# Optimization experiments

Measured on AMD Instinct MI355X. Metric: run time of the kernel, lower is better.

The kernel has to match this reference:

```python
import jax, jax.numpy as jnp
import numpy as np

B, SQ, SK, D, H = 8, 1024, 1024, 1024, 16
DH = D // H  # attention head size = 64
LN_EPS = 1e-5


def _layer_norm(x, g, b):
    m = jnp.mean(x, axis=-1, keepdims=True)
    v = jnp.mean(jnp.square(x - m), axis=-1, keepdims=True)
    return (x - m) * jax.lax.rsqrt(v + LN_EPS) * g + b


def setup_inputs() -> dict:
    key = jax.random.key(0)
    ks = jax.random.split(key, 12)
    s = 0.02
    return {
        "hidden_states": jax.random.normal(ks[0], (B, SQ, D), jnp.float32),
        "context": jax.random.normal(ks[1], (B, SK, D), jnp.float32),
        "Wq": jax.random.normal(ks[2], (D, D), jnp.float32) * s,
        "bq": jnp.zeros((D,), jnp.float32),
        "Wk": jax.random.normal(ks[3], (D, D), jnp.float32) * s,
        "bk": jnp.zeros((D,), jnp.float32),
        "Wv": jax.random.normal(ks[4], (D, D), jnp.float32) * s,
        "bv": jnp.zeros((D,), jnp.float32),
        "Wobs": jax.random.normal(ks[5], (D, D), jnp.float32) * s,
        "bobs": jnp.zeros((D,), jnp.float32),
        "Wmat": jax.random.normal(ks[6], (D, D), jnp.float32) * s,
        "bmat": jnp.zeros((D,), jnp.float32),
        "ln_g": jnp.ones((D,), jnp.float32),
        "ln_b": jnp.zeros((D,), jnp.float32),
    }


def reference(hidden_states, context, Wq, bq, Wk, bk, Wv, bv,
              Wobs, bobs, Wmat, bmat, ln_g, ln_b):
    # QKV projections (torch Linear: x @ W.T + b)
    q = hidden_states @ Wq.T + bq            # [B, SQ, D]
    k = context @ Wk.T + bk                  # [B, SK, D]
    v = context @ Wv.T + bv                  # [B, SK, D]

    # ---- Guide_Block: single-head SDPA over full D, then linear->ReLU->LN ----
    # (dropout is identity in eval mode)
    score = jnp.einsum('bqd,bkd->bqk', q, k) / np.sqrt(D)   # [B, SQ, SK]
    attn = jax.nn.softmax(score, axis=-1)
    gctx = jnp.einsum('bqk,bkd->bqd', attn, v)              # [B, SQ, D]
    new_q = _layer_norm(jax.nn.relu(gctx @ Wobs.T + bobs), ln_g, ln_b)
    new_k = _layer_norm(jax.nn.relu(k @ Wmat.T + bmat), ln_g, ln_b)

    # ---- Multi-head attention with guided q/k and original v ----
    qh = new_q.reshape(B, SQ, H, DH).transpose(0, 2, 1, 3)  # [B, H, SQ, DH]
    kh = new_k.reshape(B, SK, H, DH).transpose(0, 2, 1, 3)
    vh = v.reshape(B, SK, H, DH).transpose(0, 2, 1, 3)
    scores = jnp.einsum('bhqd,bhkd->bhqk', qh, kh) / np.sqrt(DH)
    probs = jax.nn.softmax(scores, axis=-1)                 # attn dropout = identity (eval)
    out = jnp.einsum('bhqk,bhkd->bhqd', probs, vh)          # [B, H, SQ, DH]
    return out.transpose(0, 2, 1, 3).reshape(B, SQ, D)
```

## Files before the change

kernel.cpp:

```cpp
#include <hip/hip_runtime.h>
#include <hip/hip_bf16.h>

#define DEV __device__ __forceinline__

using bf16x8 = __attribute__((ext_vector_type(8))) short;
using f32x4  = __attribute__((ext_vector_type(4))) float;

#define MFMA16(a, b, c) __builtin_amdgcn_mfma_f32_16x16x32_bf16((a), (b), (c), 0, 0, 0)

#define GLOAD_LDS16(gp, lp)                                                        \
  __builtin_amdgcn_global_load_lds(                                               \
      (__attribute__((address_space(1))) unsigned int*)(gp),                      \
      (__attribute__((address_space(3))) unsigned int*)(lp), 16, 0, 0)

DEV float b2f(unsigned short u) {
  union { float f; unsigned u; } x; x.u = ((unsigned)u) << 16; return x.f;
}
DEV unsigned short f2b(float f) {
  union { float f; unsigned u; } x; x.f = f;
  unsigned r = x.u + 0x7FFFu + ((x.u >> 16) & 1u);
  return (unsigned short)(r >> 16);
}
DEV unsigned short f2b_trunc(float f) {
  union { float f; unsigned u; } x; x.f = f;
  return (unsigned short)(x.u >> 16);
}

__global__ __launch_bounds__(256) void detect_kernel(
    const unsigned short* __restrict__ hs, int* __restrict__ flag) {
  __shared__ int red[4];
  const int t = threadIdx.x;
  const ushort4* p = (const ushort4*)hs;
  int cnt = 0;
#pragma unroll
  for (int j = 0; j < 16; j++) {
    ushort4 u = p[j * 256 + t];
    cnt += (((u.x >> 7) & 0xFF) == 0xFF) + (((u.y >> 7) & 0xFF) == 0xFF) +
           (((u.z >> 7) & 0xFF) == 0xFF) + (((u.w >> 7) & 0xFF) == 0xFF);
  }
#pragma unroll
  for (int off = 32; off >= 1; off >>= 1) cnt += __shfl_xor(cnt, off, 64);
  if ((t & 63) == 0) red[t >> 6] = cnt;
  __syncthreads();
  if (t == 0) flag[0] = (red[0] + red[1] + red[2] + red[3] >= 4) ? 1 : 0;
}

__global__ __launch_bounds__(256) void convert2_kernel(
    const void* __restrict__ s0, const void* __restrict__ s1,
    unsigned short* __restrict__ d0, unsigned short* __restrict__ d1,
    const int* __restrict__ flag) {
  const int bid = blockIdx.x;
  const void* src;
  unsigned short* dst;
  long off;
  if (bid < 8192) { src = s0; dst = d0; off = (long)bid * 1024; }
  else            { src = s1; dst = d1; off = (long)(bid - 8192) * 1024; }
  const long i = off + threadIdx.x * 4;
  ushort4 o;
  if (*flag) {
    float4 f = ((const float4*)src)[i >> 2];
    o.x = f2b(f.x); o.y = f2b(f.y); o.z = f2b(f.z); o.w = f2b(f.w);
  } else {
    o = ((const ushort4*)src)[i >> 2];
  }
  ((ushort4*)dst)[i >> 2] = o;
}

__global__ __launch_bounds__(256) void convert_w_kernel(
    const void* __restrict__ s0, const void* __restrict__ s1,
    const void* __restrict__ s2, const void* __restrict__ s3,
    const void* __restrict__ s4, unsigned short* __restrict__ dst,
    const int* __restrict__ flag) {
  const void* srcs[5] = {s0, s1, s2, s3, s4};
  const void* src = srcs[blockIdx.y];
  unsigned short* d = dst + (long)blockIdx.y * 1048576;
  const int i = (blockIdx.x * 256 + threadIdx.x) * 4;
  ushort4 o;
  if (*flag) {
    float4 f = ((const float4*)src)[i >> 2];
    o.x = f2b(f.x); o.y = f2b(f.y); o.z = f2b(f.z); o.w = f2b(f.w);
  } else {
    o = ((const ushort4*)src)[i >> 2];
  }
  ((ushort4*)d)[i >> 2] = o;
}

__global__ __launch_bounds__(256) void convert_vec_kernel(
    const void* __restrict__ s0, const void* __restrict__ s1,
    const void* __restrict__ s2, const void* __restrict__ s3,
    const void* __restrict__ s4, const void* __restrict__ s5,
    const void* __restrict__ s6, unsigned short* __restrict__ dst,
    const int* __restrict__ flag) {
  const void* srcs[7] = {s0, s1, s2, s3, s4, s5, s6};
  const void* src = srcs[blockIdx.x];
  unsigned short* d = dst + blockIdx.x * 1024;
  const int i = threadIdx.x * 4;
  ushort4 o;
  if (*flag) {
    float4 f = ((const float4*)src)[i >> 2];
    o.x = f2b(f.x); o.y = f2b(f.y); o.z = f2b(f.z); o.w = f2b(f.w);
  } else {
    o = ((const ushort4*)src)[i >> 2];
  }
  ((ushort4*)d)[i >> 2] = o;
}

template <int RELU, int OUTBF16, int BIAS, int SPLIT>
__global__ __launch_bounds__(256, 2) void gemm_bt_kernel(
    const unsigned short* __restrict__ A, const unsigned short* __restrict__ B,
    const unsigned short* __restrict__ bias, void* __restrict__ Cv,
    void* __restrict__ Cv2, int M, int N, int K, long sA_, long sB_, long sC_,
    float scale) {
  __shared__ unsigned short sA[2][128 * 32];
  __shared__ unsigned short sB[2][128 * 32];
  const int t = threadIdx.x;
  const int wave = t >> 6, lane = t & 63;
  const int quad = lane >> 4, col = lane & 15;
  const int wm = wave >> 1, wn = wave & 1;
  const long zb = blockIdx.z;
  const unsigned short* Ab = A + zb * sA_ + (long)blockIdx.x * 128 * K;
  const unsigned short* Bb = B + zb * sB_ + (long)blockIdx.y * 128 * K;
  const int r0 = t >> 2;
  const int c0 = (t & 3) * 8;

  f32x4 zz = {0.f, 0.f, 0.f, 0.f};
  f32x4 acc[4][4];
#pragma unroll
  for (int i = 0; i < 4; i++)
#pragma unroll
    for (int j = 0; j < 4; j++) acc[i][j] = zz;

  for (int k0 = 0; k0 < K; k0 += 64) {
    __syncthreads();
#pragma unroll
    for (int p = 0; p < 2; p++) {
      GLOAD_LDS16(Ab + (long)r0 * K + k0 + p * 32 + c0,        &sA[p][t * 8]);
      GLOAD_LDS16(Ab + (long)(64 + r0) * K + k0 + p * 32 + c0, &sA[p][2048 + t * 8]);
      GLOAD_LDS16(Bb + (long)r0 * K + k0 + p * 32 + c0,        &sB[p][t * 8]);
      GLOAD_LDS16(Bb + (long)(64 + r0) * K + k0 + p * 32 + c0, &sB[p][2048 + t * 8]);
    }
    __syncthreads();
#pragma unroll
    for (int p = 0; p < 2; p++) {
      bf16x8 af[4], bfr[4];
#pragma unroll
      for (int mi = 0; mi < 4; mi++)
        af[mi] = *(const bf16x8*)&sA[p][(wm * 64 + mi * 16 + col) * 32 + quad * 8];
#pragma unroll
      for (int ni = 0; ni < 4; ni++)
        bfr[ni] = *(const bf16x8*)&sB[p][(wn * 64 + ni * 16 + col) * 32 + quad * 8];
#pragma unroll
      for (int mi = 0; mi < 4; mi++)
#pragma unroll
        for (int ni = 0; ni < 4; ni++)
          acc[mi][ni] = MFMA16(af[mi], bfr[ni], acc[mi][ni]);
    }
  }

  const int Rm = blockIdx.x * 128 + wm * 64;
  const int Cn = blockIdx.y * 128 + wn * 64;
  float bs[4];
#pragma unroll
  for (int ni = 0; ni < 4; ni++)
    bs[ni] = BIAS ? b2f(bias[Cn + ni * 16 + col]) : 0.f;

  unsigned short* Cb = (unsigned short*)Cv;
  int Nw = N, cadj = 0;
  if (SPLIT) {
    Nw = N >> 1;
    if (blockIdx.y >= (gridDim.y >> 1)) { Cb = (unsigned short*)Cv2; cadj = Nw; }
  }
#pragma unroll
  for (int mi = 0; mi < 4; mi++)
#pragma unroll
    for (int ni = 0; ni < 4; ni++)
#pragma unroll
      for (int r = 0; r < 4; r++) {
        int rr = Rm + mi * 16 + quad * 4 + r;
        int cc = Cn + ni * 16 + col;
        float v = acc[mi][ni][r] * scale + bs[ni];
        if (RELU) v = fmaxf(v, 0.f);
        if (OUTBF16)
          Cb[zb * sC_ + (long)rr * Nw + (cc - cadj)] = f2b(v);
        else
          ((float*)Cv)[zb * sC_ + (long)rr * N + cc] = v;
      }
}

__global__ __launch_bounds__(256) void softmax_kernel(
    const float* __restrict__ S, unsigned short* __restrict__ P) {
  __shared__ float red[8];
  const long row = blockIdx.x;
  const int t = threadIdx.x;
  const float4 v4 = ((const float4*)(S + row * 1024))[t];
  float x[4] = {v4.x, v4.y, v4.z, v4.w};
  float m = fmaxf(fmaxf(x[0], x[1]), fmaxf(x[2], x[3]));
#pragma unroll
  for (int off = 32; off >= 1; off >>= 1) m = fmaxf(m, __shfl_xor(m, off, 64));
  if ((t & 63) == 0) red[t >> 6] = m;
  __syncthreads();
  m = fmaxf(fmaxf(red[0], red[1]), fmaxf(red[2], red[3]));
  float e[4], s = 0.f;
#pragma unroll
  for (int i = 0; i < 4; i++) { e[i] = __expf(x[i] - m); s += e[i]; }
#pragma unroll
  for (int off = 32; off >= 1; off >>= 1) s += __shfl_xor(s, off, 64);
  __syncthreads();
  if ((t & 63) == 0) red[4 + (t >> 6)] = s;
  __syncthreads();
  s = red[4] + red[5] + red[6] + red[7];
  float inv = 1.f / s;
  ushort4 o;
  o.x = f2b(e[0] * inv); o.y = f2b(e[1] * inv);
  o.z = f2b(e[2] * inv); o.w = f2b(e[3] * inv);
  ((ushort4*)(P + row * 1024))[t] = o;
}

DEV float block_sum(float v, float* red, int t) {
#pragma unroll
  for (int off = 32; off >= 1; off >>= 1) v += __shfl_xor(v, off, 64);
  __syncthreads();
  if ((t & 63) == 0) red[t >> 6] = v;
  __syncthreads();
  return red[0] + red[1] + red[2] + red[3];
}

__global__ __launch_bounds__(256) void layernorm2_kernel(
    const unsigned short* __restrict__ X0, const unsigned short* __restrict__ X1,
    const unsigned short* __restrict__ G, const unsigned short* __restrict__ Bt,
    unsigned short* __restrict__ Y0, unsigned short* __restrict__ Y1) {
  __shared__ float red[4];
  const int bid = blockIdx.x;
  const unsigned short* X;
  unsigned short* Y;
  if (bid < 8192) { X = X0 + (long)bid * 1024; Y = Y0 + (long)bid * 1024; }
  else { X = X1 + (long)(bid - 8192) * 1024; Y = Y1 + (long)(bid - 8192) * 1024; }
  const int t = threadIdx.x;
  ushort4 u = ((const ushort4*)X)[t];
  float x[4] = {b2f(u.x), b2f(u.y), b2f(u.z), b2f(u.w)};
  float s = x[0] + x[1] + x[2] + x[3];
  float mean = block_sum(s, red, t) * (1.f / 1024.f);
  float d0 = x[0] - mean, d1 = x[1] - mean, d2 = x[2] - mean, d3 = x[3] - mean;
  float vs = d0 * d0 + d1 * d1 + d2 * d2 + d3 * d3;
  float var = block_sum(vs, red, t) * (1.f / 1024.f);
  float rs = rsqrtf(var + 1e-5f);
  ushort4 gu = ((const ushort4*)G)[t];
  ushort4 bu = ((const ushort4*)Bt)[t];
  ushort4 o;
  o.x = f2b(d0 * rs * b2f(gu.x) + b2f(bu.x));
  o.y = f2b(d1 * rs * b2f(gu.y) + b2f(bu.y));
  o.z = f2b(d2 * rs * b2f(gu.z) + b2f(bu.z));
  o.w = f2b(d3 * rs * b2f(gu.w) + b2f(bu.w));
  ((ushort4*)Y)[t] = o;
}

__global__ __launch_bounds__(256) void transpose_kernel(
    const unsigned short* __restrict__ V, unsigned short* __restrict__ VT) {
  __shared__ unsigned short tile[32][33];
  const int b = blockIdx.z;
  const int d0 = blockIdx.x * 32, sk0 = blockIdx.y * 32;
  const int tx = threadIdx.x & 31, ty = threadIdx.x >> 5;
#pragma unroll
  for (int i = 0; i < 32; i += 8)
    tile[ty + i][tx] = V[((long)(b * 1024 + sk0 + ty + i)) * 1024 + d0 + tx];
  __syncthreads();
#pragma unroll
  for (int i = 0; i < 32; i += 8)
    VT[((long)(b * 1024 + d0 + ty + i)) * 1024 + sk0 + tx] = tile[tx][ty + i];
}

__global__ __launch_bounds__(256, 2) void flash_mha_kernel(
    const unsigned short* __restrict__ Q, const unsigned short* __restrict__ K,
    const unsigned short* __restrict__ VT, void* __restrict__ O,
    const int* __restrict__ flag) {
  __shared__ unsigned short sK[2][2][32 * 32];
  __shared__ unsigned short sV[2][64 * 32];
  __shared__ unsigned short sP[4][32 * 32];
  const int t = threadIdx.x;
  const int wave = t >> 6, lane = t & 63;
  const int quad = lane >> 4, col = lane & 15;
  const int b = blockIdx.z, h = blockIdx.y;
  const int q0 = blockIdx.x * 128 + wave * 32;

  const int h2 = t >> 7, i7 = t & 127;
  const unsigned short* Ksrc =
      K + ((long)(b * 1024 + (i7 >> 2))) * 1024 + h * 64 + h2 * 32 + (i7 & 3) * 8;
  const unsigned short* Vsrc =
      VT + ((long)(b * 1024 + h * 64 + (t >> 2))) * 1024 + (t & 3) * 8;

  bf16x8 aq[2][2];
  {
    const unsigned short* qp =
        Q + ((long)(b * 1024 + q0 + col)) * 1024 + h * 64 + quad * 8;
    aq[0][0] = *(const bf16x8*)(qp);
    aq[0][1] = *(const bf16x8*)(qp + 32);
    aq[1][0] = *(const bf16x8*)(qp + 16 * 1024);
    aq[1][1] = *(const bf16x8*)(qp + 16 * 1024 + 32);
  }

  const f32x4 zz = {0.f, 0.f, 0.f, 0.f};
  f32x4 o[2][4], l[2];
#pragma unroll
  for (int mt = 0; mt < 2; mt++) {
    l[mt] = zz;
#pragma unroll
    for (int n = 0; n < 4; n++) o[mt][n] = zz;
  }
  bf16x8 ones;
#pragma unroll
  for (int i = 0; i < 8; i++) ones[i] = (short)0x3F80;

#define STAGE_KV(bi, kv0)                                             \
  {                                                                   \
    GLOAD_LDS16(Ksrc + (long)(kv0) * 1024, &sK[bi][h2][i7 * 8]);      \
    GLOAD_LDS16(Vsrc + (kv0), &sV[bi][t * 8]);                        \
  }

  STAGE_KV(0, 0);
  unsigned short* pw = &sP[wave][0];
  for (int kt = 0; kt < 32; kt++) {
    const int bi = kt & 1;
    __syncthreads();
    if (kt < 31) STAGE_KV(bi ^ 1, (kt + 1) * 32);

    bf16x8 kf[2][2];
#pragma unroll
    for (int nt = 0; nt < 2; nt++)
#pragma unroll
      for (int kh = 0; kh < 2; kh++)
        kf[nt][kh] = *(const bf16x8*)&sK[bi][kh][(nt * 16 + col) * 32 + quad * 8];
    f32x4 s[2][2];
#pragma unroll
    for (int mt = 0; mt < 2; mt++)
#pragma unroll
      for (int nt = 0; nt < 2; nt++) {
        s[mt][nt] = MFMA16(aq[mt][0], kf[nt][0], zz);
        s[mt][nt] = MFMA16(aq[mt][1], kf[nt][1], s[mt][nt]);
      }
#pragma unroll
    for (int mt = 0; mt < 2; mt++)
#pragma unroll
      for (int nt = 0; nt < 2; nt++)
#pragma unroll
        for (int r = 0; r < 4; r++) {
          float p = __expf(s[mt][nt][r] * 0.125f);
          pw[(mt * 16 + quad * 4 + r) * 32 + nt * 16 + col] = f2b_trunc(p);
        }
    __asm__ __volatile__("s_waitcnt lgkmcnt(0)" ::: "memory");
    bf16x8 ap[2];
#pragma unroll
    for (int mt = 0; mt < 2; mt++)
      ap[mt] = *(const bf16x8*)&pw[(mt * 16 + col) * 32 + quad * 8];
#pragma unroll
    for (int mt = 0; mt < 2; mt++) l[mt] = MFMA16(ap[mt], ones, l[mt]);
    bf16x8 vf[4];
#pragma unroll
    for (int n = 0; n < 4; n++)
      vf[n] = *(const bf16x8*)&sV[bi][(n * 16 + col) * 32 + quad * 8];
#pragma unroll
    for (int mt = 0; mt < 2; mt++)
#pragma unroll
      for (int n = 0; n < 4; n++) o[mt][n] = MFMA16(ap[mt], vf[n], o[mt][n]);
  }
#undef STAGE_KV

  const int f32o = *flag;
#pragma unroll
  for (int mt = 0; mt < 2; mt++)
#pragma unroll
    for (int r = 0; r < 4; r++) {
      float inv = 1.f / l[mt][r];
      const long base =
          ((long)(b * 1024 + q0 + mt * 16 + quad * 4 + r)) * 1024 + h * 64 + col;
      if (f32o) {
        float* Of = (float*)O;
#pragma unroll
        for (int n = 0; n < 4; n++) Of[base + n * 16] = o[mt][n][r] * inv;
      } else {
        unsigned short* Ou = (unsigned short*)O;
#pragma unroll
        for (int n = 0; n < 4; n++) Ou[base + n * 16] = f2b(o[mt][n][r] * inv);
      }
    }
}

extern "C" void kernel_launch(void* const* d_in, const int* in_sizes, int n_in,
                              void* d_out, int out_size, void* d_ws,
                              size_t ws_size, hipStream_t stream) {
  (void)in_sizes; (void)n_in; (void)out_size; (void)ws_size;
  const void* hs   = d_in[0];
  const void* ctx  = d_in[1];
  const void* Wq   = d_in[2];
  const void* bq   = d_in[3];
  const void* Wk   = d_in[4];
  const void* bk   = d_in[5];
  const void* Wv   = d_in[6];
  const void* bv   = d_in[7];
  const void* Wobs = d_in[8];
  const void* bobs = d_in[9];
  const void* Wmat = d_in[10];
  const void* bmat = d_in[11];
  const void* lng  = d_in[12];
  const void* lnb  = d_in[13];

  const long E = 8LL * 1024 * 1024;
  const long W1 = 1024L * 1024L;
  unsigned short* base = (unsigned short*)d_ws;
  unsigned short* hsb   = base;
  unsigned short* ctxb  = base + E;
  unsigned short* Wb    = base + 2 * E;
  unsigned short* Wqb   = Wb;
  unsigned short* Wkb   = Wb + W1;
  unsigned short* Wvb   = Wb + 2 * W1;
  unsigned short* Wobsb = Wb + 3 * W1;
  unsigned short* Wmatb = Wb + 4 * W1;
  unsigned short* vecs  = base + 2 * E + 5 * W1;
  unsigned short* bqb   = vecs;
  unsigned short* bkb   = vecs + 1024;
  unsigned short* bvb   = vecs + 2048;
  unsigned short* bobsb = vecs + 3072;
  unsigned short* bmatb = vecs + 4096;
  unsigned short* lngb  = vecs + 5120;
  unsigned short* lnbb  = vecs + 6144;
  int* flag = (int*)(vecs + 32768);
  unsigned short* q     = vecs + W1;
  unsigned short* k     = q + E;
  unsigned short* v     = k + E;
  unsigned short* vT    = v + E;
  float* scores = (float*)(vT + E);
  unsigned short* nq    = (unsigned short*)scores;
  unsigned short* newq  = ((unsigned short*)scores) + E;
  unsigned short* probs = hsb;
  unsigned short* gctx  = ctxb;
  unsigned short* nk    = v;
  unsigned short* newk  = q;

  dim3 blk(256);
  const long S1 = 1024L * 1024L;

  detect_kernel<<<dim3(1), blk, 0, stream>>>((const unsigned short*)hs, flag);
  convert2_kernel<<<dim3(16384), blk, 0, stream>>>(hs, ctx, hsb, ctxb, flag);
  convert_w_kernel<<<dim3(1024, 5), blk, 0, stream>>>(Wq, Wk, Wv, Wobs, Wmat, Wb, flag);
  convert_vec_kernel<<<dim3(7), blk, 0, stream>>>(bq, bk, bv, bobs, bmat, lng, lnb,
                                                  vecs, flag);

  gemm_bt_kernel<0, 1, 1, 0><<<dim3(64, 8, 1), blk, 0, stream>>>(
      hsb, Wqb, bqb, q, q, 8192, 1024, 1024, 0, 0, 0, 1.f);
  gemm_bt_kernel<0, 1, 1, 1><<<dim3(64, 16, 1), blk, 0, stream>>>(
      ctxb, Wkb, bkb, k, v, 8192, 2048, 1024, 0, 0, 0, 1.f);
  transpose_kernel<<<dim3(32, 32, 8), blk, 0, stream>>>(v, vT);
  gemm_bt_kernel<0, 0, 0, 0><<<dim3(8, 8, 8), blk, 0, stream>>>(
      q, k, nullptr, scores, scores, 1024, 1024, 1024, S1, S1, S1, 0.03125f);
  softmax_kernel<<<dim3(8192), blk, 0, stream>>>(scores, probs);
  gemm_bt_kernel<0, 1, 0, 0><<<dim3(8, 8, 8), blk, 0, stream>>>(
      probs, vT, nullptr, gctx, gctx, 1024, 1024, 1024, S1, S1, S1, 1.f);
  gemm_bt_kernel<1, 1, 1, 0><<<dim3(64, 8, 1), blk, 0, stream>>>(
      gctx, Wobsb, bobsb, nq, nq, 8192, 1024, 1024, 0, 0, 0, 1.f);
  gemm_bt_kernel<1, 1, 1, 0><<<dim3(64, 8, 1), blk, 0, stream>>>(
      k, Wmatb, bmatb, nk, nk, 8192, 1024, 1024, 0, 0, 0, 1.f);
  layernorm2_kernel<<<dim3(16384), blk, 0, stream>>>(nq, nk, lngb, lnbb, newq, newk);
  flash_mha_kernel<<<dim3(8, 16, 8), blk, 0, stream>>>(
      newq, newk, vT, d_out, flag);
}
```

Baseline: 405.4 us.

## Compute V transposed directly via swapped GEMM and widen flash MHA query tile

The separate V projection and transpose kernel are replaced by a GEMM that computes W_v·ctx^T, writing V^T per batch with a row-wise bias, which removes one full read and write pass over V. The flash multi-head attention kernel now handles 64 query rows per wave (256 per block) instead of 32, so each staged K/V tile is reused across twice as many queries. The P scratch buffer gets padded rows. The cost is higher register pressure in the flash kernel and half as many blocks, which may lower occupancy. The GEMM template is also reworked into mode-based epilogues.

```diff
diff --git a/kernel.cpp b/kernel.cpp
--- a/kernel.cpp
+++ b/kernel.cpp
@@ -105,12 +105,11 @@
   ((ushort4*)d)[i >> 2] = o;
 }
 
-template <int RELU, int OUTBF16, int BIAS, int SPLIT>
+template <int MODE>
 __global__ __launch_bounds__(256, 2) void gemm_bt_kernel(
     const unsigned short* __restrict__ A, const unsigned short* __restrict__ B,
-    const unsigned short* __restrict__ bias, void* __restrict__ Cv,
-    void* __restrict__ Cv2, int M, int N, int K, long sA_, long sB_, long sC_,
-    float scale) {
+    const void* __restrict__ aux, void* __restrict__ Cv,
+    int M, int N, int K, long sA_, long sB_, long sC_, float scale) {
   __shared__ unsigned short sA[2][128 * 32];
   __shared__ unsigned short sB[2][128 * 32];
   const int t = threadIdx.x;
@@ -159,32 +158,39 @@
 
   const int Rm = blockIdx.x * 128 + wm * 64;
   const int Cn = blockIdx.y * 128 + wn * 64;
-  float bs[4];
-#pragma unroll
-  for (int ni = 0; ni < 4; ni++)
-    bs[ni] = BIAS ? b2f(bias[Cn + ni * 16 + col]) : 0.f;
-
-  unsigned short* Cb = (unsigned short*)Cv;
-  int Nw = N, cadj = 0;
-  if (SPLIT) {
-    Nw = N >> 1;
-    if (blockIdx.y >= (gridDim.y >> 1)) { Cb = (unsigned short*)Cv2; cadj = Nw; }
-  }
-#pragma unroll
-  for (int mi = 0; mi < 4; mi++)
+  float bs[4] = {0.f, 0.f, 0.f, 0.f};
+  if (MODE == 0 || MODE == 1) {
 #pragma unroll
     for (int ni = 0; ni < 4; ni++)
+      bs[ni] = b2f(((const unsigned short*)aux)[Cn + ni * 16 + col]);
+  }
+#pragma unroll
+  for (int mi = 0; mi < 4; mi++) {
+    float rowf[4];
+#pragma unroll
+    for (int r = 0; r < 4; r++) {
+      const int rr = Rm + mi * 16 + quad * 4 + r;
+      rowf[r] = (MODE == 4) ? b2f(((const unsigned short*)aux)[rr]) : 0.f;
+    }
+#pragma unroll
+    for (int ni = 0; ni < 4; ni++)
 #pragma unroll
       for (int r = 0; r < 4; r++) {
-        int rr = Rm + mi * 16 + quad * 4 + r;
-        int cc = Cn + ni * 16 + col;
-        float v = acc[mi][ni][r] * scale + bs[ni];
-        if (RELU) v = fmaxf(v, 0.f);
-        if (OUTBF16)
-          Cb[zb * sC_ + (long)rr * Nw + (cc - cadj)] = f2b(v);
+        const int rr = Rm + mi * 16 + quad * 4 + r;
+        const int cc = Cn + ni * 16 + col;
+        float v = acc[mi][ni][r] * scale;
+        if (MODE == 0 || MODE == 1) v += bs[ni];
+        if (MODE == 1) v = fmaxf(v, 0.f);
+        if (MODE == 4) v += rowf[r];
+        if (MODE == 2)
+          ((float*)Cv)[zb * sC_ + (long)rr * N + cc] = v;
+        else if (MODE == 4)
+          ((unsigned short*)Cv)[(long)(cc >> 10) * 1048576 + (long)rr * 1024 +
+                                (cc & 1023)] = f2b(v);
         else
-          ((float*)Cv)[zb * sC_ + (long)rr * N + cc] = v;
+          ((unsigned short*)Cv)[zb * sC_ + (long)rr * N + cc] = f2b(v);
       }
+  }
 }
 
 __global__ __launch_bounds__(256) void softmax_kernel(
@@ -254,33 +260,18 @@
   ((ushort4*)Y)[t] = o;
 }
 
-__global__ __launch_bounds__(256) void transpose_kernel(
-    const unsigned short* __restrict__ V, unsigned short* __restrict__ VT) {
-  __shared__ unsigned short tile[32][33];
-  const int b = blockIdx.z;
-  const int d0 = blockIdx.x * 32, sk0 = blockIdx.y * 32;
-  const int tx = threadIdx.x & 31, ty = threadIdx.x >> 5;
-#pragma unroll
-  for (int i = 0; i < 32; i += 8)
-    tile[ty + i][tx] = V[((long)(b * 1024 + sk0 + ty + i)) * 1024 + d0 + tx];
-  __syncthreads();
-#pragma unroll
-  for (int i = 0; i < 32; i += 8)
-    VT[((long)(b * 1024 + d0 + ty + i)) * 1024 + sk0 + tx] = tile[tx][ty + i];
-}
-
 __global__ __launch_bounds__(256, 2) void flash_mha_kernel(
     const unsigned short* __restrict__ Q, const unsigned short* __restrict__ K,
     const unsigned short* __restrict__ VT, void* __restrict__ O,
     const int* __restrict__ flag) {
   __shared__ unsigned short sK[2][2][32 * 32];
   __shared__ unsigned short sV[2][64 * 32];
-  __shared__ unsigned short sP[4][32 * 32];
+  __shared__ unsigned short sP[4][64 * 40];
   const int t = threadIdx.x;
   const int wave = t >> 6, lane = t & 63;
   const int quad = lane >> 4, col = lane & 15;
   const int b = blockIdx.z, h = blockIdx.y;
-  const int q0 = blockIdx.x * 128 + wave * 32;
+  const int q0 = blockIdx.x * 256 + wave * 64;
 
   const int h2 = t >> 7, i7 = t & 127;
   const unsigned short* Ksrc =
@@ -288,20 +279,21 @@
   const unsigned short* Vsrc =
       VT + ((long)(b * 1024 + h * 64 + (t >> 2))) * 1024 + (t & 3) * 8;
 
-  bf16x8 aq[2][2];
+  bf16x8 aq[4][2];
   {
     const unsigned short* qp =
         Q + ((long)(b * 1024 + q0 + col)) * 1024 + h * 64 + quad * 8;
-    aq[0][0] = *(const bf16x8*)(qp);
-    aq[0][1] = *(const bf16x8*)(qp + 32);
-    aq[1][0] = *(const bf16x8*)(qp + 16 * 1024);
-    aq[1][1] = *(const bf16x8*)(qp + 16 * 1024 + 32);
+#pragma unroll
+    for (int mt = 0; mt < 4; mt++) {
+      aq[mt][0] = *(const bf16x8*)(qp + (long)mt * 16 * 1024);
+      aq[mt][1] = *(const bf16x8*)(qp + (long)mt * 16 * 1024 + 32);
+    }
   }
 
   const f32x4 zz = {0.f, 0.f, 0.f, 0.f};
-  f32x4 o[2][4], l[2];
-#pragma unroll
-  for (int mt = 0; mt < 2; mt++) {
+  f32x4 o[4][4], l[4];
+#pragma unroll
+  for (int mt = 0; mt < 4; mt++) {
     l[mt] = zz;
 #pragma unroll
     for (int n = 0; n < 4; n++) o[mt][n] = zz;
@@ -329,36 +321,36 @@
 #pragma unroll
       for (int kh = 0; kh < 2; kh++)
         kf[nt][kh] = *(const bf16x8*)&sK[bi][kh][(nt * 16 + col) * 32 + quad * 8];
-    f32x4 s[2][2];
-#pragma unroll
-    for (int mt = 0; mt < 2; mt++)
+    f32x4 s[4][2];
+#pragma unroll
+    for (int mt = 0; mt < 4; mt++)
 #pragma unroll
       for (int nt = 0; nt < 2; nt++) {
         s[mt][nt] = MFMA16(aq[mt][0], kf[nt][0], zz);
         s[mt][nt] = MFMA16(aq[mt][1], kf[nt][1], s[mt][nt]);
       }
 #pragma unroll
-    for (int mt = 0; mt < 2; mt++)
+    for (int mt = 0; mt < 4; mt++)
 #pragma unroll
       for (int nt = 0; nt < 2; nt++)
 #pragma unroll
         for (int r = 0; r < 4; r++) {
           float p = __expf(s[mt][nt][r] * 0.125f);
-          pw[(mt * 16 + quad * 4 + r) * 32 + nt * 16 + col] = f2b_trunc(p);
+          pw[(mt * 16 + quad * 4 + r) * 40 + nt * 16 + col] = f2b_trunc(p);
         }
     __asm__ __volatile__("s_waitcnt lgkmcnt(0)" ::: "memory");
-    bf16x8 ap[2];
-#pragma unroll
-    for (int mt = 0; mt < 2; mt++)
-      ap[mt] = *(const bf16x8*)&pw[(mt * 16 + col) * 32 + quad * 8];
-#pragma unroll
-    for (int mt = 0; mt < 2; mt++) l[mt] = MFMA16(ap[mt], ones, l[mt]);
+    bf16x8 ap[4];
+#pragma unroll
+    for (int mt = 0; mt < 4; mt++)
+      ap[mt] = *(const bf16x8*)&pw[(mt * 16 + col) * 40 + quad * 8];
+#pragma unroll
+    for (int mt = 0; mt < 4; mt++) l[mt] = MFMA16(ap[mt], ones, l[mt]);
     bf16x8 vf[4];
 #pragma unroll
     for (int n = 0; n < 4; n++)
       vf[n] = *(const bf16x8*)&sV[bi][(n * 16 + col) * 32 + quad * 8];
 #pragma unroll
-    for (int mt = 0; mt < 2; mt++)
+    for (int mt = 0; mt < 4; mt++)
 #pragma unroll
       for (int n = 0; n < 4; n++) o[mt][n] = MFMA16(ap[mt], vf[n], o[mt][n]);
   }
@@ -366,7 +358,7 @@
 
   const int f32o = *flag;
 #pragma unroll
-  for (int mt = 0; mt < 2; mt++)
+  for (int mt = 0; mt < 4; mt++)
 #pragma unroll
     for (int r = 0; r < 4; r++) {
       float inv = 1.f / l[mt][r];
@@ -425,15 +417,16 @@
   int* flag = (int*)(vecs + 32768);
   unsigned short* q     = vecs + W1;
   unsigned short* k     = q + E;
-  unsigned short* v     = k + E;
-  unsigned short* vT    = v + E;
-  float* scores = (float*)(vT + E);
-  unsigned short* nq    = (unsigned short*)scores;
-  unsigned short* newq  = ((unsigned short*)scores) + E;
+  unsigned short* vT    = k + E;
+  unsigned short* N1    = vT + E;
+  unsigned short* N2    = N1 + E;
+  float* scores = (float*)(N2 + E);
   unsigned short* probs = hsb;
   unsigned short* gctx  = ctxb;
-  unsigned short* nk    = v;
-  unsigned short* newk  = q;
+  unsigned short* nq    = N1;
+  unsigned short* nk    = q;
+  unsigned short* newq  = (unsigned short*)scores;
+  unsigned short* newk  = N2;
 
   dim3 blk(256);
   const long S1 = 1024L * 1024L;
@@ -444,21 +437,22 @@
   convert_vec_kernel<<<dim3(7), blk, 0, stream>>>(bq, bk, bv, bobs, bmat, lng, lnb,
                                                   vecs, flag);
 
-  gemm_bt_kernel<0, 1, 1, 0><<<dim3(64, 8, 1), blk, 0, stream>>>(
-      hsb, Wqb, bqb, q, q, 8192, 1024, 1024, 0, 0, 0, 1.f);
-  gemm_bt_kernel<0, 1, 1, 1><<<dim3(64, 16, 1), blk, 0, stream>>>(
-      ctxb, Wkb, bkb, k, v, 8192, 2048, 1024, 0, 0, 0, 1.f);
-  transpose_kernel<<<dim3(32, 32, 8), blk, 0, stream>>>(v, vT);
-  gemm_bt_kernel<0, 0, 0, 0><<<dim3(8, 8, 8), blk, 0, stream>>>(
-      q, k, nullptr, scores, scores, 1024, 1024, 1024, S1, S1, S1, 0.03125f);
+  gemm_bt_kernel<0><<<dim3(64, 8, 1), blk, 0, stream>>>(
+      hsb, Wqb, bqb, q, 8192, 1024, 1024, 0, 0, 0, 1.f);
+  gemm_bt_kernel<0><<<dim3(64, 8, 1), blk, 0, stream>>>(
+      ctxb, Wkb, bkb, k, 8192, 1024, 1024, 0, 0, 0, 1.f);
+  gemm_bt_kernel<4><<<dim3(8, 64, 1), blk, 0, stream>>>(
+      Wvb, ctxb, bvb, vT, 1024, 8192, 1024, 0, 0, 0, 1.f);
+  gemm_bt_kernel<2><<<dim3(8, 8, 8), blk, 0, stream>>>(
+      q, k, nullptr, scores, 1024, 1024, 1024, S1, S1, S1, 0.03125f);
   softmax_kernel<<<dim3(8192), blk, 0, stream>>>(scores, probs);
-  gemm_bt_kernel<0, 1, 0, 0><<<dim3(8, 8, 8), blk, 0, stream>>>(
-      probs, vT, nullptr, gctx, gctx, 1024, 1024, 1024, S1, S1, S1, 1.f);
-  gemm_bt_kernel<1, 1, 1, 0><<<dim3(64, 8, 1), blk, 0, stream>>>(
-      gctx, Wobsb, bobsb, nq, nq, 8192, 1024, 1024, 0, 0, 0, 1.f);
-  gemm_bt_kernel<1, 1, 1, 0><<<dim3(64, 8, 1), blk, 0, stream>>>(
-      k, Wmatb, bmatb, nk, nk, 8192, 1024, 1024, 0, 0, 0, 1.f);
+  gemm_bt_kernel<3><<<dim3(8, 8, 8), blk, 0, stream>>>(
+      probs, vT, nullptr, gctx, 1024, 1024, 1024, S1, S1, S1, 1.f);
+  gemm_bt_kernel<1><<<dim3(64, 8, 1), blk, 0, stream>>>(
+      gctx, Wobsb, bobsb, nq, 8192, 1024, 1024, 0, 0, 0, 1.f);
+  gemm_bt_kernel<1><<<dim3(64, 8, 1), blk, 0, stream>>>(
+      k, Wmatb, bmatb, nk, 8192, 1024, 1024, 0, 0, 0, 1.f);
   layernorm2_kernel<<<dim3(16384), blk, 0, stream>>>(nq, nk, lngb, lnbb, newq, newk);
-  flash_mha_kernel<<<dim3(8, 16, 8), blk, 0, stream>>>(
+  flash_mha_kernel<<<dim3(4, 16, 8), blk, 0, stream>>>(
       newq, newk, vT, d_out, flag);
 }
```

New measurement: 406.3 us. No clear change (+0.2%).
